# Performance work log

Hardware: AMD Instinct MI355X
Metric: run time of the kernel (lower is better)

Reference implementation:

```python
import jax, jax.numpy as jnp
import numpy as np

N_NODES = 50000
N_EDGES = 640000
RAW = 128
HID = 256
COORD = 3


def setup_inputs() -> dict:
    key = jax.random.key(0)
    ks = jax.random.split(key, 20)

    def w(k, fan_in, fan_out):
        return (jax.random.normal(k, (fan_in, fan_out), jnp.float32)
                / np.float32(np.sqrt(fan_in)))

    return {
        "edge_index": jax.random.randint(ks[0], (2, N_EDGES), 0, N_NODES, jnp.int64)
        if jax.config.jax_enable_x64 else
        jax.random.randint(ks[0], (2, N_EDGES), 0, N_NODES, jnp.int32),
        "str_feature": jax.random.normal(ks[1], (N_NODES, RAW), jnp.float32),
        "coord_feature": jax.random.normal(ks[2], (N_NODES, COORD), jnp.float32),
        # msg_mlp: Linear(2*RAW+1 -> HID), SiLU, Linear(HID -> HID), SiLU
        "msg_w1": w(ks[3], 2 * RAW + 1, HID), "msg_b1": jnp.zeros((HID,), jnp.float32),
        "msg_w2": w(ks[4], HID, HID), "msg_b2": jnp.zeros((HID,), jnp.float32),
        # trans_mlp: Linear(HID->HID), SiLU, Linear(HID->HID), SiLU, Linear(HID->1, no bias, xavier gain=0.001)
        "tr_w1": w(ks[5], HID, HID), "tr_b1": jnp.zeros((HID,), jnp.float32),
        "tr_w2": w(ks[6], HID, HID), "tr_b2": jnp.zeros((HID,), jnp.float32),
        "tr_w3": w(ks[7], HID, 1) * np.float32(0.001),
        # posi_mlp: Linear(RAW+HID->HID), SiLU, Linear(HID->RAW)
        "posi_w1": w(ks[8], RAW + HID, HID), "posi_b1": jnp.zeros((HID,), jnp.float32),
        "posi_w2": w(ks[9], HID, RAW), "posi_b2": jnp.zeros((RAW,), jnp.float32),
    }


def reference(edge_index, str_feature, coord_feature,
              msg_w1, msg_b1, msg_w2, msg_b2,
              tr_w1, tr_b1, tr_w2, tr_b2, tr_w3,
              posi_w1, posi_b1, posi_w2, posi_b2):
    silu = jax.nn.silu
    row, col = edge_index[0], edge_index[1]
    n = str_feature.shape[0]

    # coord2dist
    coord_diff = coord_feature[row] - coord_feature[col]          # [E, 3]
    sqr_dist = jnp.sum(coord_diff * coord_diff, axis=1, keepdims=True)  # [E, 1]

    # msg_model
    edge_in = jnp.concatenate([str_feature[row], str_feature[col], sqr_dist], axis=1)
    msg = silu(silu(edge_in @ msg_w1 + msg_b1) @ msg_w2 + msg_b2)  # [E, HID]

    # coord_model: trans = coord_diff * trans_mlp(msg); x += segment_mean(trans, row)
    gate = silu(silu(msg @ tr_w1 + tr_b1) @ tr_w2 + tr_b2) @ tr_w3  # [E, 1]
    trans = coord_diff * gate                                       # [E, 3]
    trans_sum = jax.ops.segment_sum(trans, row, num_segments=n)     # [N, 3]
    cnt = jax.ops.segment_sum(jnp.ones((trans.shape[0],), trans.dtype), row,
                              num_segments=n)
    trans_mean = trans_sum / jnp.clip(cnt, 1.0)[:, None]
    coord_out = coord_feature + trans_mean

    # posi_model: p + posi_mlp([p, segment_sum(msg, row)])
    msg_sum = jax.ops.segment_sum(msg, row, num_segments=n)         # [N, HID]
    p_in = jnp.concatenate([str_feature, msg_sum], axis=1)
    str_out = str_feature + (silu(p_in @ posi_w1 + posi_b1) @ posi_w2 + posi_b2)

    return str_out, coord_out
```

## Files before the change

### kernel.cpp

```cpp
#include <hip/hip_runtime.h>

#define NN 50000
#define NE 640000

typedef __bf16 bf16x8 __attribute__((ext_vector_type(8)));
typedef short  short8 __attribute__((ext_vector_type(8)));
typedef float  f32x16 __attribute__((ext_vector_type(16)));
typedef float  f32x2  __attribute__((ext_vector_type(2)));
typedef float  f32x4  __attribute__((ext_vector_type(4)));

__device__ __forceinline__ short f2bf(float v) {
  unsigned u = __builtin_bit_cast(unsigned, v);
  u = (u + 0x7FFFu + ((u >> 16) & 1u)) >> 16;
  return (short)u;
}
__device__ __forceinline__ short f2bf_hw(float v) {
  return __builtin_bit_cast(short, (__bf16)v);
}
__device__ __forceinline__ unsigned pack2(float a, float b) {
  return (unsigned)(unsigned short)f2bf_hw(a) | ((unsigned)(unsigned short)f2bf_hw(b) << 16);
}
__device__ __forceinline__ float silu_f(float v) {
  float e = __builtin_amdgcn_exp2f(v * -1.44269504f);
  return v * __builtin_amdgcn_rcpf(1.0f + e);
}
__device__ __forceinline__ bf16x8 ld8(const short* p) {
  return *(const bf16x8*)(p);
}
__device__ __forceinline__ void atomic_add_f(float* p, float v) {
  __hip_atomic_fetch_add(p, v, __ATOMIC_RELAXED, __HIP_MEMORY_SCOPE_AGENT);
}

__global__ void egcl_prep(const float* __restrict__ mw1, const float* __restrict__ mb1,
                          const float* __restrict__ mw2, const float* __restrict__ mb2,
                          const float* __restrict__ tw1, const float* __restrict__ tb1,
                          const float* __restrict__ tw2, const float* __restrict__ tb2,
                          const float* __restrict__ pw1, const float* __restrict__ pw2,
                          const float* __restrict__ strf, const int* __restrict__ rowp,
                          short* __restrict__ w1t, short* __restrict__ w2t,
                          short* __restrict__ t1t, short* __restrict__ t2t,
                          short* __restrict__ p1t, short* __restrict__ p2t,
                          short* __restrict__ strb, int* __restrict__ deg)
{
  const int S0 = 71680, S2 = 98304, S3 = 32768, SS = NN * 128;
  const int total = 4 * S0 + S2 + S3 + SS + NE;
  int stride = gridDim.x * blockDim.x;
  for (int i = blockIdx.x * blockDim.x + threadIdx.x; i < total; i += stride) {
    int j = i;
    if (j < S0) { int n = j / 280, k = j - n * 280;
      float v = (k < 257) ? mw1[k * 256 + n] : ((k == 257) ? mb1[n] : 0.0f);
      w1t[j] = f2bf(v); continue; }
    j -= S0;
    if (j < S0) { int n = j / 280, k = j - n * 280;
      float v = (k < 256) ? mw2[k * 256 + n] : ((k == 257) ? mb2[n] : 0.0f);
      w2t[j] = f2bf(v); continue; }
    j -= S0;
    if (j < S0) { int n = j / 280, k = j - n * 280;
      float v = (k < 256) ? tw1[k * 256 + n] : ((k == 257) ? tb1[n] : 0.0f);
      t1t[j] = f2bf(v); continue; }
    j -= S0;
    if (j < S0) { int n = j / 280, k = j - n * 280;
      float v = (k < 256) ? tw2[k * 256 + n] : ((k == 257) ? tb2[n] : 0.0f);
      t2t[j] = f2bf(v); continue; }
    j -= S0;
    if (j < S2) { int n = j / 384, k = j - n * 384; p1t[j] = f2bf(pw1[k * 256 + n]); continue; }
    j -= S2;
    if (j < S3) { int n = j >> 8, k = j & 255; p2t[j] = f2bf(pw2[k * 128 + n]); continue; }
    j -= S3;
    if (j < SS) { strb[j] = f2bf(strf[j]); continue; }
    j -= SS;
    atomicAdd(deg + rowp[j], 1);
  }
}

__global__ __launch_bounds__(1024)
void egcl_scan(const int* __restrict__ deg, int* __restrict__ base)
{
  __shared__ int wsum[16], wincl[16];
  __shared__ int carry_s;
  const int tid = threadIdx.x, lane = tid & 63, w = tid >> 6;
  if (tid == 0) carry_s = 0;
  __syncthreads();
  for (int start = 0; start < NN; start += 1024) {
    const int i = start + tid;
    int v = (i < NN) ? deg[i] : 0;
    int s = v;
#pragma unroll
    for (int off = 1; off < 64; off <<= 1) {
      int t = __shfl_up(s, off);
      if (lane >= off) s += t;
    }
    if (lane == 63) wsum[w] = s;
    __syncthreads();
    if (w == 0) {
      int u = (lane < 16) ? wsum[lane] : 0;
#pragma unroll
      for (int off = 1; off < 16; off <<= 1) {
        int t = __shfl_up(u, off);
        if (lane >= off) u += t;
      }
      if (lane < 16) wincl[lane] = u;
    }
    __syncthreads();
    const int waveoff = wincl[w] - wsum[w];
    const int carry = carry_s;
    if (i < NN) base[i] = carry + waveoff + s - v;
    __syncthreads();
    if (tid == 0) carry_s = carry + wincl[15];
    __syncthreads();
  }
  if (tid == 0) base[NN] = NE;
}

__global__ void egcl_scatter(const int* __restrict__ rowp, const int* __restrict__ base,
                             int* __restrict__ cursor, int* __restrict__ eidg)
{
  int stride = gridDim.x * blockDim.x;
  for (int e = blockIdx.x * blockDim.x + threadIdx.x; e < NE; e += stride) {
    int r = rowp[e];
    int pos = base[r] + atomicAdd(cursor + r, 1);
    eidg[pos] = e;
  }
}


__device__ __forceinline__ void gemm32(const short* Ab, const short* __restrict__ WT,
                                       int wn, int nh, int lh, int l32,
                                       f32x16 acc[2])
{
  acc[0] = (f32x16)(0.0f); acc[1] = (f32x16)(0.0f);
  const short* arow = Ab + l32 * 280 + lh * 8;
  const short* brow = WT + (wn * 64 + nh * 32 + l32) * 280 + lh * 8;
#pragma unroll
  for (int ks = 0; ks < 17; ++ks) {
    const int kb = ks * 16;
    bf16x8 b  = ld8(brow + kb);
    bf16x8 a0 = ld8(arow + kb);
    bf16x8 a1 = ld8(arow + 32 * 280 + kb);
    acc[0] = __builtin_amdgcn_mfma_f32_32x32x16_bf16(a0, b, acc[0], 0, 0, 0);
    acc[1] = __builtin_amdgcn_mfma_f32_32x32x16_bf16(a1, b, acc[1], 0, 0, 0);
  }
}

__device__ __forceinline__ void comp_pack32(const f32x16 acc[2], unsigned pk[16])
{
#pragma unroll
  for (int sm = 0; sm < 2; ++sm)
#pragma unroll
    for (int j = 0; j < 8; ++j) {
      float v0 = silu_f(acc[sm][2 * j]);
      float v1 = silu_f(acc[sm][2 * j + 1]);
      pk[sm * 8 + j] = pack2(v0, v1);
    }
}

__device__ __forceinline__ void write_pk32(short* Ab, const unsigned pk0[16],
                                           const unsigned pk1[16],
                                           int wn, int lh, int l32)
{
#pragma unroll
  for (int nh = 0; nh < 2; ++nh) {
    const unsigned* pk = nh ? pk1 : pk0;
    const int n = wn * 64 + nh * 32 + l32;
#pragma unroll
    for (int sm = 0; sm < 2; ++sm) {
      short* dst = Ab + (sm * 32 + 4 * lh) * 280 + n;
#pragma unroll
      for (int j = 0; j < 8; ++j) {
        const int row = (j & 1) * 2 + 8 * (j >> 1);
        const unsigned u = pk[sm * 8 + j];
        dst[row * 280]       = (short)(u & 0xFFFFu);
        dst[(row + 1) * 280] = (short)(u >> 16);
      }
    }
  }
}

__global__ __launch_bounds__(256, 4)
void egcl_edge(const int* __restrict__ eidx, const float* __restrict__ coord,
               const short* __restrict__ strb, const int* __restrict__ eidg,
               const int* __restrict__ base,
               const short* __restrict__ w1t, const short* __restrict__ w2t,
               const short* __restrict__ t1t, const short* __restrict__ t2t,
               const float* __restrict__ tr_w3,
               float* __restrict__ msg_sum, float* __restrict__ trans_sum)
{
  __shared__ short Ab[64 * 280];
  __shared__ int   rs_s[64], cs_s[64], own_s[64];
  __shared__ float cdx_s[64], cdy_s[64], cdz_s[64], gate_s[64];

  const int tid  = threadIdx.x;
  const int lane = tid & 63, wave = tid >> 6;
  const int lh = lane >> 5, l32 = lane & 31;
  const int wn = wave;
  const int p0 = blockIdx.x * 64;
  const int* __restrict__ rowp = eidx;
  const int* __restrict__ colp = eidx + NE;

  if (tid < 64) {
    int e = eidg[p0 + tid];
    int r = rowp[e], c = colp[e];
    rs_s[tid] = r; cs_s[tid] = c;
    const int wstart = p0 + (tid & ~31);
    own_s[tid] = (base[r] >= wstart) && (base[r + 1] <= wstart + 32) ? 1 : 0;
    float dx = coord[r * 3 + 0] - coord[c * 3 + 0];
    float dy = coord[r * 3 + 1] - coord[c * 3 + 1];
    float dz = coord[r * 3 + 2] - coord[c * 3 + 2];
    cdx_s[tid] = dx; cdy_s[tid] = dy; cdz_s[tid] = dz;
    short8 d8 = (short8)(short)0;
    d8[0] = f2bf(dx * dx + dy * dy + dz * dz);
    d8[1] = f2bf(1.0f);
    *(short8*)(Ab + tid * 280 + 256) = d8;
    *(short8*)(Ab + tid * 280 + 264) = (short8)(short)0;
    *(short8*)(Ab + tid * 280 + 272) = (short8)(short)0;
  }
  __syncthreads();
#pragma unroll
  for (int it = 0; it < 8; ++it) {
    int i = tid + it * 256;
    int e = i >> 5, cc = i & 31;
    int node = (cc < 16) ? rs_s[e] : cs_s[e];
    short8 v = *(const short8*)(strb + node * 128 + (cc & 15) * 8);
    *(short8*)(Ab + e * 280 + cc * 8) = v;
  }
  __syncthreads();

  f32x16 acc[2];
  unsigned pk0[16], pk1[16];

  gemm32(Ab, w1t, wn, 0, lh, l32, acc);
  comp_pack32(acc, pk0);
  gemm32(Ab, w1t, wn, 1, lh, l32, acc);
  comp_pack32(acc, pk1);
  __syncthreads();
  write_pk32(Ab, pk0, pk1, wn, lh, l32);
  __syncthreads();

  gemm32(Ab, w2t, wn, 0, lh, l32, acc);
  comp_pack32(acc, pk0);
  gemm32(Ab, w2t, wn, 1, lh, l32, acc);
  comp_pack32(acc, pk1);
  __syncthreads();
  write_pk32(Ab, pk0, pk1, wn, lh, l32);
  __syncthreads();

  gemm32(Ab, t1t, wn, 0, lh, l32, acc);
  comp_pack32(acc, pk0);
  gemm32(Ab, t1t, wn, 1, lh, l32, acc);
  comp_pack32(acc, pk1);
  {
    const int cp  = tid & 127;
    const int e0w = (tid >> 7) * 32;
    float run0 = 0.0f, run1 = 0.0f;
    int prev = rs_s[e0w];
    int own  = own_s[e0w];
#pragma unroll 4
    for (int i = 0; i < 32; ++i) {
      const int idx = e0w + i;
      const int r = rs_s[idx];
      unsigned u = *(const unsigned*)(Ab + idx * 280 + cp * 2);
      float lo = __builtin_bit_cast(float, u << 16);
      float hi = __builtin_bit_cast(float, u & 0xFFFF0000u);
      if (r != prev) {
        if (own) {
          f32x2 v; v.x = run0; v.y = run1;
          *((f32x2*)msg_sum + prev * 128 + cp) = v;
        } else {
          atomic_add_f(msg_sum + prev * 256 + cp * 2 + 0, run0);
          atomic_add_f(msg_sum + prev * 256 + cp * 2 + 1, run1);
        }
        run0 = 0.0f; run1 = 0.0f; prev = r; own = own_s[idx];
      }
      run0 += lo; run1 += hi;
    }
    if (own) {
      f32x2 v; v.x = run0; v.y = run1;
      *((f32x2*)msg_sum + prev * 128 + cp) = v;
    } else {
      atomic_add_f(msg_sum + prev * 256 + cp * 2 + 0, run0);
      atomic_add_f(msg_sum + prev * 256 + cp * 2 + 1, run1);
    }
  }
  __syncthreads();
  write_pk32(Ab, pk0, pk1, wn, lh, l32);
  __syncthreads();

  gemm32(Ab, t2t, wn, 0, lh, l32, acc);
  comp_pack32(acc, pk0);
  gemm32(Ab, t2t, wn, 1, lh, l32, acc);
  comp_pack32(acc, pk1);
  __syncthreads();
  write_pk32(Ab, pk0, pk1, wn, lh, l32);
  __syncthreads();

  {
    const int e = tid >> 2, p = tid & 3;
    const short* ap = Ab + e * 280 + p * 64;
    const float4* wp = (const float4*)(tr_w3 + p * 64);
    float s = 0.0f;
#pragma unroll
    for (int j = 0; j < 8; ++j) {
      bf16x8 av = ld8(ap + j * 8);
      float4 w0 = wp[2 * j], w1 = wp[2 * j + 1];
      s += (float)av[0] * w0.x + (float)av[1] * w0.y + (float)av[2] * w0.z + (float)av[3] * w0.w;
      s += (float)av[4] * w1.x + (float)av[5] * w1.y + (float)av[6] * w1.z + (float)av[7] * w1.w;
    }
    s += __shfl_xor(s, 1);
    s += __shfl_xor(s, 2);
    if (p == 0) gate_s[e] = s;
  }
  __syncthreads();
  if (tid < 3) {
    const int c = tid;
    float run = 0.0f;
    int prev = rs_s[0];
    for (int i = 0; i < 64; ++i) {
      const int r = rs_s[i];
      if (r != prev) { atomic_add_f(trans_sum + prev * 3 + c, run); run = 0.0f; prev = r; }
      const float cd = (c == 0) ? cdx_s[i] : ((c == 1) ? cdy_s[i] : cdz_s[i]);
      run += cd * gate_s[i];
    }
    atomic_add_f(trans_sum + prev * 3 + c, run);
  }
}

__global__ __launch_bounds__(256, 3)
void egcl_node(const float* __restrict__ strf, const float* __restrict__ coord,
               const short* __restrict__ strb,
               const short* __restrict__ p1t, const short* __restrict__ p2t,
               const float* __restrict__ pb1, const float* __restrict__ pb2,
               const float* __restrict__ msg_sum, const float* __restrict__ trans_sum,
               const int* __restrict__ base, float* __restrict__ out)
{
  __shared__ short Ab[64 * 392];
  const int tid  = threadIdx.x;
  const int lane = tid & 63, wave = tid >> 6;
  const int quad = lane >> 4, l16 = lane & 15;
  const int n0 = blockIdx.x * 64;

#pragma unroll
  for (int it = 0; it < 4; ++it) {
    int i = tid + it * 256;
    int m = i >> 4, c = i & 15;
    int n = n0 + m;
    short8 v = (short8)(short)0;
    if (n < NN) v = *(const short8*)(strb + n * 128 + c * 8);
    *(short8*)(Ab + m * 392 + c * 8) = v;
  }
#pragma unroll
  for (int it = 0; it < 8; ++it) {
    int i = tid + it * 256;
    int m = i >> 5, c = i & 31;
    int n = n0 + m;
    short8 v = (short8)(short)0;
    if (n < NN) {
      const float* src = msg_sum + n * 256 + c * 8;
#pragma unroll
      for (int j = 0; j < 8; ++j) v[j] = f2bf_hw(src[j]);
    }
    *(short8*)(Ab + m * 392 + 128 + c * 8) = v;
  }
  __syncthreads();

  f32x4 acc[4][4];
#pragma unroll
  for (int nt = 0; nt < 4; ++nt)
#pragma unroll
    for (int mt = 0; mt < 4; ++mt) acc[nt][mt] = (f32x4)(0.0f);
#pragma unroll
  for (int ks = 0; ks < 12; ++ks) {
    const int kb = ks * 32 + quad * 8;
    bf16x8 b[4];
#pragma unroll
    for (int nt = 0; nt < 4; ++nt)
      b[nt] = ld8(p1t + (wave * 64 + nt * 16 + l16) * 384 + kb);
#pragma unroll
    for (int mt = 0; mt < 4; ++mt) {
      bf16x8 a = ld8(Ab + (mt * 16 + l16) * 392 + kb);
#pragma unroll
      for (int nt = 0; nt < 4; ++nt)
        acc[nt][mt] = __builtin_amdgcn_mfma_f32_16x16x32_bf16(a, b[nt], acc[nt][mt], 0, 0, 0);
    }
  }
  __syncthreads();
#pragma unroll
  for (int nt = 0; nt < 4; ++nt) {
    const int n = wave * 64 + nt * 16 + l16;
    const float bn = pb1[n];
#pragma unroll
    for (int mt = 0; mt < 4; ++mt)
#pragma unroll
      for (int r = 0; r < 4; ++r) {
        const int m = mt * 16 + quad * 4 + r;
        Ab[m * 392 + n] = f2bf_hw(silu_f(acc[nt][mt][r] + bn));
      }
  }
  __syncthreads();

  f32x4 a2[2][4];
#pragma unroll
  for (int nt = 0; nt < 2; ++nt)
#pragma unroll
    for (int mt = 0; mt < 4; ++mt) a2[nt][mt] = (f32x4)(0.0f);
#pragma unroll
  for (int ks = 0; ks < 8; ++ks) {
    const int kb = ks * 32 + quad * 8;
    bf16x8 b0 = ld8(p2t + (wave * 32 + l16) * 256 + kb);
    bf16x8 b1 = ld8(p2t + (wave * 32 + 16 + l16) * 256 + kb);
#pragma unroll
    for (int mt = 0; mt < 4; ++mt) {
      bf16x8 a = ld8(Ab + (mt * 16 + l16) * 392 + kb);
      a2[0][mt] = __builtin_amdgcn_mfma_f32_16x16x32_bf16(a, b0, a2[0][mt], 0, 0, 0);
      a2[1][mt] = __builtin_amdgcn_mfma_f32_16x16x32_bf16(a, b1, a2[1][mt], 0, 0, 0);
    }
  }
#pragma unroll
  for (int nt = 0; nt < 2; ++nt) {
    const int c = wave * 32 + nt * 16 + l16;
    const float bc = pb2[c];
#pragma unroll
    for (int mt = 0; mt < 4; ++mt)
#pragma unroll
      for (int r = 0; r < 4; ++r) {
        const int m = mt * 16 + quad * 4 + r;
        const int n = n0 + m;
        if (n < NN) out[n * 128 + c] = strf[n * 128 + c] + a2[nt][mt][r] + bc;
      }
  }
  if (tid < 64) {
    const int n = n0 + tid;
    if (n < NN) {
      float cv = (float)(base[n + 1] - base[n]); if (cv < 1.0f) cv = 1.0f;
      float inv = __builtin_amdgcn_rcpf(cv);
      out[NN * 128 + n * 3 + 0] = coord[n * 3 + 0] + trans_sum[n * 3 + 0] * inv;
      out[NN * 128 + n * 3 + 1] = coord[n * 3 + 1] + trans_sum[n * 3 + 1] * inv;
      out[NN * 128 + n * 3 + 2] = coord[n * 3 + 2] + trans_sum[n * 3 + 2] * inv;
    }
  }
}

extern "C" void kernel_launch(void* const* d_in, const int* in_sizes, int n_in,
                              void* d_out, int out_size, void* d_ws, size_t ws_size,
                              hipStream_t stream)
{
  const int*   eidx   = (const int*)d_in[0];
  const float* strf   = (const float*)d_in[1];
  const float* coord  = (const float*)d_in[2];
  const float* msg_w1 = (const float*)d_in[3];
  const float* msg_b1 = (const float*)d_in[4];
  const float* msg_w2 = (const float*)d_in[5];
  const float* msg_b2 = (const float*)d_in[6];
  const float* tr_w1  = (const float*)d_in[7];
  const float* tr_b1  = (const float*)d_in[8];
  const float* tr_w2  = (const float*)d_in[9];
  const float* tr_b2  = (const float*)d_in[10];
  const float* tr_w3  = (const float*)d_in[11];
  const float* posi_w1 = (const float*)d_in[12];
  const float* posi_b1 = (const float*)d_in[13];
  const float* posi_w2 = (const float*)d_in[14];
  const float* posi_b2 = (const float*)d_in[15];
  float* out = (float*)d_out;

  char* ws = (char*)d_ws;
  float* msg_sum   = (float*)ws;
  float* trans_sum = msg_sum + NN * 256;
  int*   deg       = (int*)(trans_sum + NN * 3);
  int*   cursor    = deg + NN;
  int*   base      = cursor + NN;
  int*   eidg      = base + NN + 8;
  short* strb = (short*)(eidg + NE);
  short* w1t  = strb + NN * 128;
  short* w2t  = w1t + 71680;
  short* t1t  = w2t + 71680;
  short* t2t  = t1t + 71680;
  short* p1t  = t2t + 71680;
  short* p2t  = p1t + 98304;

  const int* rowp = eidx;

  (void)hipMemsetAsync(ws, 0, (size_t)(NN * 256 + NN * 3 + NN + NN) * 4, stream);
  egcl_prep<<<2048, 256, 0, stream>>>(msg_w1, msg_b1, msg_w2, msg_b2,
                                      tr_w1, tr_b1, tr_w2, tr_b2,
                                      posi_w1, posi_w2,
                                      strf, rowp, w1t, w2t, t1t, t2t, p1t, p2t, strb, deg);
  egcl_scan<<<1, 1024, 0, stream>>>(deg, base);
  egcl_scatter<<<2560, 256, 0, stream>>>(rowp, base, cursor, eidg);
  egcl_edge<<<NE / 64, 256, 0, stream>>>(eidx, coord, strb, eidg, base,
                                         w1t, w2t, t1t, t2t, tr_w3,
                                         msg_sum, trans_sum);
  egcl_node<<<(NN + 63) / 64, 256, 0, stream>>>(strf, coord, strb, p1t, p2t,
                                                posi_b1, posi_b2,
                                                msg_sum, trans_sum, base, out);
}
```

Measured before the change: 976.3 us.

## Replace single-block degree scan with three-pass multi-block scan

The exclusive prefix sum over node degrees previously ran in one 1024-thread block that looped serially over 49 chunks. It is now split into a reduce-then-scan-then-propagate sequence: per-block sums, a single small block scanning the 98 partials, and a parallel pass writing the final offsets. This targets the latency of the serial single-block scan, at the cost of two extra kernel launches and a small workspace area for the partials.

```diff
diff --git a/kernel.cpp b/kernel.cpp
--- a/kernel.cpp
+++ b/kernel.cpp
@@ -73,43 +73,74 @@
   }
 }
 
-__global__ __launch_bounds__(1024)
-void egcl_scan(const int* __restrict__ deg, int* __restrict__ base)
-{
-  __shared__ int wsum[16], wincl[16];
-  __shared__ int carry_s;
+#define SCB ((NN + 511) / 512)
+
+__global__ __launch_bounds__(512)
+void egcl_scan_a(const int* __restrict__ deg, int* __restrict__ psum)
+{
+  __shared__ int ws[8];
   const int tid = threadIdx.x, lane = tid & 63, w = tid >> 6;
-  if (tid == 0) carry_s = 0;
-  __syncthreads();
-  for (int start = 0; start < NN; start += 1024) {
-    const int i = start + tid;
-    int v = (i < NN) ? deg[i] : 0;
-    int s = v;
-#pragma unroll
-    for (int off = 1; off < 64; off <<= 1) {
-      int t = __shfl_up(s, off);
-      if (lane >= off) s += t;
-    }
-    if (lane == 63) wsum[w] = s;
+  const int i = blockIdx.x * 512 + tid;
+  int s = (i < NN) ? deg[i] : 0;
+#pragma unroll
+  for (int off = 1; off < 64; off <<= 1) s += __shfl_xor(s, off);
+  if (lane == 0) ws[w] = s;
+  __syncthreads();
+  if (tid == 0) {
+    int t = 0;
+#pragma unroll
+    for (int k = 0; k < 8; ++k) t += ws[k];
+    psum[blockIdx.x] = t;
+  }
+}
+
+__global__ __launch_bounds__(128)
+void egcl_scan_b(const int* __restrict__ psum, int* __restrict__ poff,
+                 int* __restrict__ base)
+{
+  __shared__ int buf[128];
+  const int tid = threadIdx.x;
+  int v = (tid < SCB) ? psum[tid] : 0;
+  buf[tid] = v;
+  __syncthreads();
+#pragma unroll
+  for (int off = 1; off < 128; off <<= 1) {
+    int t = (tid >= off) ? buf[tid - off] : 0;
     __syncthreads();
-    if (w == 0) {
-      int u = (lane < 16) ? wsum[lane] : 0;
-#pragma unroll
-      for (int off = 1; off < 16; off <<= 1) {
-        int t = __shfl_up(u, off);
-        if (lane >= off) u += t;
-      }
-      if (lane < 16) wincl[lane] = u;
-    }
+    buf[tid] += t;
     __syncthreads();
-    const int waveoff = wincl[w] - wsum[w];
-    const int carry = carry_s;
-    if (i < NN) base[i] = carry + waveoff + s - v;
-    __syncthreads();
-    if (tid == 0) carry_s = carry + wincl[15];
-    __syncthreads();
-  }
+  }
+  if (tid < SCB) poff[tid] = buf[tid] - v;
   if (tid == 0) base[NN] = NE;
+}
+
+__global__ __launch_bounds__(512)
+void egcl_scan_c(const int* __restrict__ deg, const int* __restrict__ poff,
+                 int* __restrict__ base)
+{
+  __shared__ int wsum[8], wincl[8];
+  const int tid = threadIdx.x, lane = tid & 63, w = tid >> 6;
+  const int i = blockIdx.x * 512 + tid;
+  const int v = (i < NN) ? deg[i] : 0;
+  int s = v;
+#pragma unroll
+  for (int off = 1; off < 64; off <<= 1) {
+    int t = __shfl_up(s, off);
+    if (lane >= off) s += t;
+  }
+  if (lane == 63) wsum[w] = s;
+  __syncthreads();
+  if (w == 0 && lane < 8) {
+    int u = wsum[lane];
+#pragma unroll
+    for (int off = 1; off < 8; off <<= 1) {
+      int t = __shfl_up(u, off);
+      if (lane >= off) u += t;
+    }
+    wincl[lane] = u;
+  }
+  __syncthreads();
+  if (i < NN) base[i] = poff[blockIdx.x] + (wincl[w] - wsum[w]) + (s - v);
 }
 
 __global__ void egcl_scatter(const int* __restrict__ rowp, const int* __restrict__ base,
@@ -475,6 +506,8 @@
   short* t2t  = t1t + 71680;
   short* p1t  = t2t + 71680;
   short* p2t  = p1t + 98304;
+  int*   psum = (int*)(p2t + 32768);
+  int*   poff = psum + 128;
 
   const int* rowp = eidx;
 
@@ -483,7 +516,9 @@
                                       tr_w1, tr_b1, tr_w2, tr_b2,
                                       posi_w1, posi_w2,
                                       strf, rowp, w1t, w2t, t1t, t2t, p1t, p2t, strb, deg);
-  egcl_scan<<<1, 1024, 0, stream>>>(deg, base);
+  egcl_scan_a<<<SCB, 512, 0, stream>>>(deg, psum);
+  egcl_scan_b<<<1, 128, 0, stream>>>(psum, poff, base);
+  egcl_scan_c<<<SCB, 512, 0, stream>>>(deg, poff, base);
   egcl_scatter<<<2560, 256, 0, stream>>>(rowp, base, cursor, eidg);
   egcl_edge<<<NE / 64, 256, 0, stream>>>(eidx, coord, strb, eidg, base,
                                          w1t, w2t, t1t, t2t, tr_w3,
```

Measured after the change: 940.5 us. -3.7%, faster.
